# Optimization experiments

Hardware: AMD Instinct MI355X
Metric: run time of the kernel (lower is better)

Reference implementation:

```python
import jax, jax.numpy as jnp
import numpy as np

P = 16; RES = 224; D = 768; L = 12; H = 12; OUT = 512
NP1 = NP2 = RES // P          # 14x14 patches
NTOK = NP1 * NP2 + 1          # 197 tokens (cls + patches)
STD = 5.0                     # gaussian_std for naclip
EPS = 1e-5


def _ln(x, w, b):
    x32 = x.astype(jnp.float32)
    m = x32.mean(-1, keepdims=True)
    v = ((x32 - m) ** 2).mean(-1, keepdims=True)
    return (((x32 - m) * jax.lax.rsqrt(v + EPS)) * w + b).astype(x.dtype)


def _quick_gelu(x):
    return x * jax.nn.sigmoid(1.702 * x)


def _gaussian_addition():
    # VisionTransformer.gaussian_window + get_attention_addition, done analytically:
    # addition[i*NP2+j, k*NP2+l] = window[k-i+NP1-1, l-j+NP2-1]
    w1, w2 = 2 * NP1 - 1, 2 * NP2 - 1
    c = 1.0 / (STD * np.sqrt(2.0))
    k1 = (-(w1 - 1) / 2.0 + np.arange(w1)) * c
    k2 = (-(w2 - 1) / 2.0 + np.arange(w2)) * c
    window = np.exp(-(k1[:, None] ** 2 + k2[None, :] ** 2))
    r = np.arange(NP1)[None, :] - np.arange(NP1)[:, None] + (NP1 - 1)  # [i,k]
    cc = np.arange(NP2)[None, :] - np.arange(NP2)[:, None] + (NP2 - 1)  # [j,l]
    A = window[r[:, None, :, None], cc[None, :, None, :]]  # (NP1,NP2,NP1,NP2)
    A = A.reshape(NP1 * NP2, NP1 * NP2)
    full = np.zeros((NTOK, NTOK), dtype=np.float32)
    full[1:, 1:] = A  # zero row/col for cls token
    return jnp.asarray(full)


def _mha_vanilla(x, wi, bi, wo, bo):
    B, N, _ = x.shape
    hd = D // H
    qkv = x @ wi.T + bi                      # [B,N,3D]
    q, k, v = jnp.split(qkv, 3, axis=-1)
    q = q.reshape(B, N, H, hd); k = k.reshape(B, N, H, hd); v = v.reshape(B, N, H, hd)
    a = jnp.einsum('bqhd,bkhd->bhqk', q, k) * (hd ** -0.5)
    a = jax.nn.softmax(a, axis=-1)
    o = jnp.einsum('bhqk,bkhd->bqhd', a, v).reshape(B, N, D)
    return o @ wo.T + bo


def _mha_naclip(x, wi, bi, wo, bo, addition):
    B, N, _ = x.shape
    hd = D // H
    qkv = x @ wi.T + bi
    _, k, v = jnp.split(qkv, 3, axis=-1)
    k = k.reshape(B, N, H, hd); v = v.reshape(B, N, H, hd)
    a = jnp.einsum('bqhd,bkhd->bhqk', k, k) * (hd ** -0.5) + addition[None, None]
    a = jax.nn.softmax(a, axis=-1)
    o = jnp.einsum('bhqk,bkhd->bqhd', a, v).reshape(B, N, D)
    return o @ wo.T + bo


def _mlp(x, fw, fb, pw, pb):
    return _quick_gelu(x @ fw.T + fb) @ pw.T + pb


def setup_inputs() -> dict:
    key = jax.random.key(0)
    ks = jax.random.split(key, 16)
    s = D ** -0.5
    rn = lambda k, shape, sc=0.02: jax.random.normal(k, shape, jnp.float32) * sc
    return {
        'x': jax.random.normal(ks[0], (32, 3, RES, RES), jnp.float32),
        'conv1_w': rn(ks[1], (D, 3, P, P)),
        'class_embedding': rn(ks[2], (D,), s),
        'pos_embedding': rn(ks[3], (NTOK, D), s),
        'ln_pre_w': jnp.ones((D,)), 'ln_pre_b': jnp.zeros((D,)),
        'in_proj_w': rn(ks[4], (L, 3 * D, D)), 'in_proj_b': rn(ks[5], (L, 3 * D)),
        'out_proj_w': rn(ks[6], (L, D, D)), 'out_proj_b': rn(ks[7], (L, D)),
        'ln1_w': jnp.ones((L, D)), 'ln1_b': jnp.zeros((L, D)),
        'ln2_w': jnp.ones((L, D)), 'ln2_b': jnp.zeros((L, D)),
        'fc_w': rn(ks[8], (L, 4 * D, D)), 'fc_b': rn(ks[9], (L, 4 * D)),
        'cproj_w': rn(ks[10], (L, D, 4 * D)), 'cproj_b': rn(ks[11], (L, D)),
        'ln_post_w': jnp.ones((D,)), 'ln_post_b': jnp.zeros((D,)),
        'proj': rn(ks[12], (D, OUT), s),
    }


def reference(x, conv1_w, class_embedding, pos_embedding, ln_pre_w, ln_pre_b,
              in_proj_w, in_proj_b, out_proj_w, out_proj_b, ln1_w, ln1_b,
              ln2_w, ln2_b, fc_w, fc_b, cproj_w, cproj_b, ln_post_w, ln_post_b, proj):
    B = x.shape[0]
    # patch embed
    h = jax.lax.conv_general_dilated(x, conv1_w, (P, P), 'VALID',
                                     dimension_numbers=('NCHW', 'OIHW', 'NCHW'))
    h = h.reshape(B, D, NP1 * NP2).transpose(0, 2, 1)           # [B,196,D]
    cls = jnp.broadcast_to(class_embedding, (B, 1, D))
    h = jnp.concatenate([cls, h], axis=1) + pos_embedding        # [B,197,D]
    h = _ln(h, ln_pre_w, ln_pre_b)
    addition = _gaussian_addition()
    # first L-1 blocks: vanilla attention
    for i in range(L - 1):
        h = h + _mha_vanilla(_ln(h, ln1_w[i], ln1_b[i]), in_proj_w[i], in_proj_b[i],
                             out_proj_w[i], out_proj_b[i])
        h = h + _mlp(_ln(h, ln2_w[i], ln2_b[i]), fc_w[i], fc_b[i], cproj_w[i], cproj_b[i])
    # last block: naclip key-key attention with gaussian addition (arch='vanilla')
    i = L - 1
    reduced = _mha_naclip(_ln(h, ln1_w[i], ln1_b[i]), in_proj_w[i], in_proj_b[i],
                          out_proj_w[i], out_proj_b[i], addition)
    final = h + reduced
    final = final + _mlp(_ln(final, ln2_w[i], ln2_b[i]), fc_w[i], fc_b[i], cproj_w[i], cproj_b[i])
    return _ln(final, ln_post_w, ln_post_b) @ proj               # [B,197,OUT]
```

## Files before the change

kernel.cpp:

```cpp
#include <hip/hip_runtime.h>
#include <hip/hip_bf16.h>
#include <math.h>

#define BATCH 32
#define NTOK  197
#define NPATCH 196
#define DMODEL 768
#define NLAYER 12
#define NHEAD 12
#define HDIM  64
#define ROWS  (BATCH*NTOK)
#define CROWS (BATCH*NPATCH)
#define DFF   3072
#define DQKV  2304
#define DOUT  512
#define NBH   (BATCH*NHEAD)

#define WOFF_IN   ((size_t)0)
#define WOFF_OUT  ((size_t)(DQKV*DMODEL))
#define WOFF_FC   (WOFF_OUT + (size_t)(DMODEL*DMODEL))
#define WOFF_CP   (WOFF_FC + (size_t)(DFF*DMODEL))
#define WTOT      (WOFF_CP + (size_t)(DMODEL*DFF))

#define WS_H    ((size_t)0)
#define WS_QKVB (WS_H + (size_t)ROWS*DMODEL)
#define WS_GB   (WS_QKVB + (size_t)ROWS*DQKV/2)
#define WS_TB   (WS_GB + (size_t)ROWS*DFF/2)
#define WS_WL   (WS_TB + (size_t)ROWS*DMODEL/2)
#define WS_PTS  (WS_WL + WTOT/2)
#define WS_ADD  (WS_PTS + (size_t)DOUT*DMODEL/2)

typedef unsigned short ushort_t;
typedef __attribute__((ext_vector_type(8))) short bf16x8;
typedef __attribute__((ext_vector_type(4))) float f32x4;

__device__ inline ushort_t bf16rn(float x) {
    uint32_t u = __builtin_bit_cast(uint32_t, x);
    uint32_t r = (u + 0x7FFFu + ((u >> 16) & 1u)) >> 16;
    return (ushort_t)r;
}

#define GLL(src, dst) __builtin_amdgcn_global_load_lds( \
    (const __attribute__((address_space(1))) void*)(src), \
    (__attribute__((address_space(3))) void*)(dst), 16, 0, 0)


__global__ void im2col_bf16_k(const float* __restrict__ x, ushort_t* __restrict__ out) {
    int idx = blockIdx.x * 256 + threadIdx.x;
    if (idx >= CROWS * DMODEL / 4) return;
    int r  = idx / (DMODEL / 4);
    int k4 = (idx - r * (DMODEL / 4)) * 4;
    int b = r / NPATCH, p = r - b * NPATCH;
    int py = p / 14, px = p - py * 14;
    int c = k4 >> 8, rem = k4 & 255, i = rem >> 4, j = rem & 15;
    const float* xp = x + (((size_t)(b * 3 + c) * 224) + py * 16 + i) * 224 + px * 16 + j;
    float4 v = *(const float4*)xp;
    ushort4 hv = {bf16rn(v.x), bf16rn(v.y), bf16rn(v.z), bf16rn(v.w)};
    *(ushort4*)(out + (size_t)r * DMODEL + k4) = hv;
}

__global__ void cvt_w_k(const float* __restrict__ W, ushort_t* __restrict__ out, int NK) {
    int idx = (blockIdx.x * 256 + threadIdx.x) * 4;
    if (idx >= NK) return;
    float4 v = *(const float4*)(W + idx);
    ushort4 hv = {bf16rn(v.x), bf16rn(v.y), bf16rn(v.z), bf16rn(v.w)};
    *(ushort4*)(out + idx) = hv;
}

__global__ void cvt_layer_k(const float* __restrict__ inW, const float* __restrict__ outW,
                            const float* __restrict__ fcW, const float* __restrict__ cpW,
                            ushort_t* __restrict__ wl) {
    size_t idx = ((size_t)blockIdx.x * 256 + threadIdx.x) * 4;
    if (idx >= WTOT) return;
    const float* src; size_t off;
    if (idx < WOFF_OUT)      { src = inW;  off = idx; }
    else if (idx < WOFF_FC)  { src = outW; off = idx - WOFF_OUT; }
    else if (idx < WOFF_CP)  { src = fcW;  off = idx - WOFF_FC; }
    else                     { src = cpW;  off = idx - WOFF_CP; }
    float4 v = *(const float4*)(src + off);
    ushort4 hv = {bf16rn(v.x), bf16rn(v.y), bf16rn(v.z), bf16rn(v.w)};
    *(ushort4*)(wl + idx) = hv;
}

__global__ void cvt_pT_k(const float* __restrict__ proj, ushort_t* __restrict__ out) {
    int idx = blockIdx.x * 256 + threadIdx.x;
    if (idx >= DOUT * DMODEL) return;
    int n = idx / DMODEL, k = idx - n * DMODEL;
    out[(size_t)n * DMODEL + k] = bf16rn(proj[(size_t)k * DOUT + n]);
}

__global__ void embed_k(const float* __restrict__ conv, const float* __restrict__ cls,
                        const float* __restrict__ pos, float* __restrict__ h) {
    int idx = blockIdx.x * 256 + threadIdx.x;
    if (idx >= ROWS * DMODEL) return;
    int r = idx / DMODEL, d = idx - r * DMODEL;
    int b = r / NTOK, tok = r - b * NTOK;
    float v = (tok == 0) ? cls[d] : conv[((size_t)(b * NPATCH + tok - 1)) * DMODEL + d];
    h[idx] = v + pos[(size_t)tok * DMODEL + d];
}

__global__ void gauss_k(float* __restrict__ add) {
    int idx = blockIdx.x * 256 + threadIdx.x;
    if (idx >= NTOK * NTOK) return;
    int i = idx / NTOK, j = idx - i * NTOK;
    float v = 0.f;
    if (i > 0 && j > 0) {
        int p = i - 1, q = j - 1;
        int di = q / 14 - p / 14;
        int dj = q % 14 - p % 14;
        v = expf(-(float)(di * di + dj * dj) * 0.02f);
    }
    add[idx] = v;
}

__global__ __launch_bounds__(256) void ln768_k(const float* __restrict__ in, float* __restrict__ out,
                                               const float* __restrict__ w, const float* __restrict__ b) {
    int row = blockIdx.x, tid = threadIdx.x;
    const float* x = in + (size_t)row * DMODEL;
    float v0 = x[tid], v1 = x[tid + 256], v2 = x[tid + 512];
    float s = v0 + v1 + v2;
    float s2 = v0 * v0 + v1 * v1 + v2 * v2;
    for (int o = 32; o > 0; o >>= 1) { s += __shfl_down(s, o); s2 += __shfl_down(s2, o); }
    __shared__ float red[8];
    int wid = tid >> 6;
    if ((tid & 63) == 0) { red[wid] = s; red[4 + wid] = s2; }
    __syncthreads();
    s  = red[0] + red[1] + red[2] + red[3];
    s2 = red[4] + red[5] + red[6] + red[7];
    float mean = s * (1.0f / 768.0f);
    float var  = s2 * (1.0f / 768.0f) - mean * mean;
    float rinv = rsqrtf(var + 1e-5f);
    float* o_ = out + (size_t)row * DMODEL;
    o_[tid]       = (v0 - mean) * rinv * w[tid]       + b[tid];
    o_[tid + 256] = (v1 - mean) * rinv * w[tid + 256] + b[tid + 256];
    o_[tid + 512] = (v2 - mean) * rinv * w[tid + 512] + b[tid + 512];
}

__global__ __launch_bounds__(256) void ln768_bf16_k(const float* __restrict__ in, ushort_t* __restrict__ out,
                                                    const float* __restrict__ w, const float* __restrict__ b) {
    int row = blockIdx.x, tid = threadIdx.x;
    const float* x = in + (size_t)row * DMODEL;
    float v0 = x[tid], v1 = x[tid + 256], v2 = x[tid + 512];
    float s = v0 + v1 + v2;
    float s2 = v0 * v0 + v1 * v1 + v2 * v2;
    for (int o = 32; o > 0; o >>= 1) { s += __shfl_down(s, o); s2 += __shfl_down(s2, o); }
    __shared__ float red[8];
    int wid = tid >> 6;
    if ((tid & 63) == 0) { red[wid] = s; red[4 + wid] = s2; }
    __syncthreads();
    s  = red[0] + red[1] + red[2] + red[3];
    s2 = red[4] + red[5] + red[6] + red[7];
    float mean = s * (1.0f / 768.0f);
    float var  = s2 * (1.0f / 768.0f) - mean * mean;
    float rinv = rsqrtf(var + 1e-5f);
    ushort_t* o_ = out + (size_t)row * DMODEL;
    o_[tid]       = bf16rn((v0 - mean) * rinv * w[tid]       + b[tid]);
    o_[tid + 256] = bf16rn((v1 - mean) * rinv * w[tid + 256] + b[tid + 256]);
    o_[tid + 512] = bf16rn((v2 - mean) * rinv * w[tid + 512] + b[tid + 512]);
}

__global__ __launch_bounds__(256) void gemm_mfma_k(
    const ushort_t* __restrict__ A, const ushort_t* __restrict__ W,
    const float* __restrict__ bias, float* __restrict__ C, ushort_t* __restrict__ OS,
    int M, int N, int K, int mode)
{
    __shared__ ushort_t As[3][128][32];
    __shared__ ushort_t Bs[3][128][32];
    int tid = threadIdx.x;
    int lane = tid & 63;
    int wave = tid >> 6;
    int wm = wave >> 1, wn = wave & 1;
    int m0 = blockIdx.x * 128, n0 = blockIdx.y * 128;

    int klen = K / gridDim.z;
    int kbeg = blockIdx.z * klen;
    int nt = klen / 32;

    f32x4 acc[4][4];
    #pragma unroll
    for (int i = 0; i < 4; ++i)
        #pragma unroll
        for (int j = 0; j < 4; ++j)
            acc[i][j] = (f32x4){0.f, 0.f, 0.f, 0.f};

    int srow = tid >> 2;
    int skq  = (((tid & 3) ^ ((tid >> 3) & 3)) * 8);
    int ar0 = m0 + srow;      if (ar0 > M - 1) ar0 = M - 1;
    int ar1 = m0 + srow + 64; if (ar1 > M - 1) ar1 = M - 1;
    const ushort_t* Ap0 = A + (size_t)ar0 * K + kbeg + skq;
    const ushort_t* Ap1 = A + (size_t)ar1 * K + kbeg + skq;
    const ushort_t* Wp0 = W + (size_t)(n0 + srow) * K + kbeg + skq;
    const ushort_t* Wp1 = W + (size_t)(n0 + srow + 64) * K + kbeg + skq;
    char* ldsA = (char*)As + tid * 16;
    char* ldsB = (char*)Bs + tid * 16;

    int fr = lane & 15, fq = lane >> 4;
    int rsl = (fq ^ ((fr >> 1) & 3)) * 8;

    #define STAGE(buf_, ko_) do {                         \
        GLL(Ap0 + (ko_), ldsA + (buf_) * 8192);           \
        GLL(Ap1 + (ko_), ldsA + (buf_) * 8192 + 4096);    \
        GLL(Wp0 + (ko_), ldsB + (buf_) * 8192);           \
        GLL(Wp1 + (ko_), ldsB + (buf_) * 8192 + 4096);    \
    } while (0)

    STAGE(0, 0);
    if (nt > 1) STAGE(1, 32);

    for (int t = 0; t < nt; ++t) {
        int cur = t % 3;
        if (t + 1 < nt) {
            asm volatile("s_waitcnt vmcnt(4)" ::: "memory");
        } else {
            asm volatile("s_waitcnt vmcnt(0)" ::: "memory");
        }
        __builtin_amdgcn_s_barrier();
        bf16x8 a[4], b[4];
        #pragma unroll
        for (int fm = 0; fm < 4; ++fm)
            a[fm] = *(const bf16x8*)&As[cur][wm * 64 + fm * 16 + fr][rsl];
        #pragma unroll
        for (int fn = 0; fn < 4; ++fn)
            b[fn] = *(const bf16x8*)&Bs[cur][wn * 64 + fn * 16 + fr][rsl];
        if (t + 2 < nt) STAGE((t + 2) % 3, (size_t)(t + 2) * 32);
        #pragma unroll
        for (int fm = 0; fm < 4; ++fm)
            #pragma unroll
            for (int fn = 0; fn < 4; ++fn)
                acc[fm][fn] = __builtin_amdgcn_mfma_f32_16x16x32_bf16(a[fm], b[fn], acc[fm][fn], 0, 0, 0);
    }
    #undef STAGE

    #pragma unroll
    for (int fn = 0; fn < 4; ++fn) {
        int ccol = n0 + wn * 64 + fn * 16 + fr;
        float bv = bias ? bias[ccol] : 0.f;
        if (mode == 3 && blockIdx.z != 0) bv = 0.f;
        #pragma unroll
        for (int fm = 0; fm < 4; ++fm) {
            int crow0 = m0 + wm * 64 + fm * 16 + fq * 4;
            #pragma unroll
            for (int j = 0; j < 4; ++j) {
                int row = crow0 + j;
                if (row < M) {
                    float v = acc[fm][fn][j] + bv;
                    if (mode == 0) {
                        C[(size_t)row * N + ccol] = v;
                    } else if (mode == 3) {
                        atomicAdd(&C[(size_t)row * N + ccol], v);
                    } else if (mode == 4) {
                        OS[(size_t)row * N + ccol] = bf16rn(v);
                    } else {
                        v = v / (1.0f + expf(-1.702f * v));
                        OS[(size_t)row * N + ccol] = bf16rn(v);
                    }
                }
            }
        }
    }
}

__global__ __launch_bounds__(512, 4) void attn_fused_k(
    const ushort_t* __restrict__ qkvb, ushort_t* __restrict__ out,
    const float* __restrict__ addition, int qoff)
{
    __shared__ ushort_t Ks[208][72];
    __shared__ ushort_t Vt[64][232];
    __shared__ ushort_t Pb[8][2][16][40];
    int tid = threadIdx.x;
    int bh = blockIdx.x;
    int b = bh / NHEAD, hh = bh - b * NHEAD;
    const ushort_t* base = qkvb + (size_t)b * NTOK * DQKV + hh * HDIM;

    int lane = tid & 63, wave = tid >> 6;
    int fr = lane & 15, fq = lane >> 4;
    int qt = blockIdx.y * 8 + wave;

    bf16x8 qf0, qf1;
    if (qt < 13) {
        int qrow = qt * 16 + fr; if (qrow > NTOK - 1) qrow = NTOK - 1;
        const ushort_t* qp = base + (size_t)qrow * DQKV + qoff + fq * 8;
        qf0 = *(const bf16x8*)qp;
        qf1 = *(const bf16x8*)(qp + 32);
    }

    {
        int tt = tid >> 4, dq = tid & 15;
        #pragma unroll
        for (int pass = 0; pass < 7; ++pass) {
            int t = pass * 32 + tt;
            if (t < 208) {
                ushort4 kv = {0, 0, 0, 0}, vv = {0, 0, 0, 0};
                if (t < NTOK) {
                    kv = *(const ushort4*)(base + (size_t)t * DQKV + DMODEL + dq * 4);
                    vv = *(const ushort4*)(base + (size_t)t * DQKV + 2 * DMODEL + dq * 4);
                }
                *(ushort4*)&Ks[t][dq * 4] = kv;
                Vt[dq * 4 + 0][t] = vv.x;
                Vt[dq * 4 + 1][t] = vv.y;
                Vt[dq * 4 + 2][t] = vv.z;
                Vt[dq * 4 + 3][t] = vv.w;
            }
        }
        for (int z = tid; z < 64 * 24; z += 512) Vt[z / 24][208 + z % 24] = 0;
    }
    __syncthreads();

    if (qt < 13) {
        int i0 = qt * 16;
        int irow = i0 + fr; if (irow > NTOK - 1) irow = NTOK - 1;

        f32x4 s[13];
        #pragma unroll
        for (int jt = 0; jt < 13; ++jt) {
            bf16x8 k0 = *(const bf16x8*)&Ks[jt * 16 + fr][fq * 8];
            bf16x8 k1 = *(const bf16x8*)&Ks[jt * 16 + fr][32 + fq * 8];
            f32x4 a = {0.f, 0.f, 0.f, 0.f};
            a = __builtin_amdgcn_mfma_f32_16x16x32_bf16(k0, qf0, a, 0, 0, 0);
            a = __builtin_amdgcn_mfma_f32_16x16x32_bf16(k1, qf1, a, 0, 0, 0);
            s[jt] = a;
        }

        float mx = -1e30f;
        #pragma unroll
        for (int jt = 0; jt < 13; ++jt) {
            int jb = jt * 16 + fq * 4;
            #pragma unroll
            for (int jj = 0; jj < 4; ++jj) {
                int j = jb + jj;
                float v = s[jt][jj] * 0.125f;
                if (addition) v += addition[irow * NTOK + (j < NTOK ? j : NTOK - 1)];
                if (j >= NTOK) v = -1e30f;
                s[jt][jj] = v;
                mx = fmaxf(mx, v);
            }
        }
        mx = fmaxf(mx, __shfl_xor(mx, 16));
        mx = fmaxf(mx, __shfl_xor(mx, 32));
        float sum = 0.f;
        #pragma unroll
        for (int jt = 0; jt < 13; ++jt)
            #pragma unroll
            for (int jj = 0; jj < 4; ++jj) {
                float e = __expf(s[jt][jj] - mx);
                s[jt][jj] = e;
                sum += e;
            }
        sum += __shfl_xor(sum, 16);
        sum += __shfl_xor(sum, 32);
        float inv = 1.0f / sum;

        f32x4 o4[4];
        #pragma unroll
        for (int dt = 0; dt < 4; ++dt) o4[dt] = (f32x4){0.f, 0.f, 0.f, 0.f};

        #define WRITE_P(st_, buf_) do {                                              \
            int jA = 2 * (st_), jB = jA + 1;                                         \
            ushort4 wa = {bf16rn(s[jA][0] * inv), bf16rn(s[jA][1] * inv),            \
                          bf16rn(s[jA][2] * inv), bf16rn(s[jA][3] * inv)};           \
            ushort4 wb = {0, 0, 0, 0};                                               \
            if (jB < 13) wb = (ushort4){bf16rn(s[jB][0] * inv), bf16rn(s[jB][1] * inv), \
                                        bf16rn(s[jB][2] * inv), bf16rn(s[jB][3] * inv)}; \
            *(ushort4*)&Pb[wave][buf_][fr][fq * 4] = wa;                             \
            *(ushort4*)&Pb[wave][buf_][fr][16 + fq * 4] = wb;                        \
        } while (0)

        WRITE_P(0, 0);
        for (int st = 0; st < 7; ++st) {
            asm volatile("s_waitcnt lgkmcnt(0)" ::: "memory");
            bf16x8 pa = *(const bf16x8*)&Pb[wave][st & 1][fr][fq * 8];
            bf16x8 vf0 = *(const bf16x8*)&Vt[0 * 16 + fr][st * 32 + fq * 8];
            bf16x8 vf1 = *(const bf16x8*)&Vt[1 * 16 + fr][st * 32 + fq * 8];
            bf16x8 vf2 = *(const bf16x8*)&Vt[2 * 16 + fr][st * 32 + fq * 8];
            bf16x8 vf3 = *(const bf16x8*)&Vt[3 * 16 + fr][st * 32 + fq * 8];
            if (st < 6) WRITE_P(st + 1, (st + 1) & 1);
            o4[0] = __builtin_amdgcn_mfma_f32_16x16x32_bf16(pa, vf0, o4[0], 0, 0, 0);
            o4[1] = __builtin_amdgcn_mfma_f32_16x16x32_bf16(pa, vf1, o4[1], 0, 0, 0);
            o4[2] = __builtin_amdgcn_mfma_f32_16x16x32_bf16(pa, vf2, o4[2], 0, 0, 0);
            o4[3] = __builtin_amdgcn_mfma_f32_16x16x32_bf16(pa, vf3, o4[3], 0, 0, 0);
        }
        #undef WRITE_P

        #pragma unroll
        for (int jj = 0; jj < 4; ++jj) {
            int ir = i0 + fq * 4 + jj;
            if (ir < NTOK) {
                ushort_t* op = out + ((size_t)(b * NTOK + ir)) * DMODEL + hh * HDIM + fr;
                #pragma unroll
                for (int dt = 0; dt < 4; ++dt)
                    op[dt * 16] = bf16rn(o4[dt][jj]);
            }
        }
    }
}

extern "C" void kernel_launch(void* const* d_in, const int* in_sizes, int n_in,
                              void* d_out, int out_size, void* d_ws, size_t ws_size,
                              hipStream_t stream) {
    const float* x        = (const float*)d_in[0];
    const float* conv1_w  = (const float*)d_in[1];
    const float* cls      = (const float*)d_in[2];
    const float* pos      = (const float*)d_in[3];
    const float* ln_pre_w = (const float*)d_in[4];
    const float* ln_pre_b = (const float*)d_in[5];
    const float* in_proj_w  = (const float*)d_in[6];
    const float* in_proj_b  = (const float*)d_in[7];
    const float* out_proj_w = (const float*)d_in[8];
    const float* out_proj_b = (const float*)d_in[9];
    const float* ln1_w = (const float*)d_in[10];
    const float* ln1_b = (const float*)d_in[11];
    const float* ln2_w = (const float*)d_in[12];
    const float* ln2_b = (const float*)d_in[13];
    const float* fc_w  = (const float*)d_in[14];
    const float* fc_b  = (const float*)d_in[15];
    const float* cproj_w = (const float*)d_in[16];
    const float* cproj_b = (const float*)d_in[17];
    const float* ln_post_w = (const float*)d_in[18];
    const float* ln_post_b = (const float*)d_in[19];
    const float* proj = (const float*)d_in[20];
    float* out = (float*)d_out;

    float* ws   = (float*)d_ws;
    float* h    = ws + WS_H;
    float* ctmp = ws + WS_QKVB;
    ushort_t* qkvb = (ushort_t*)(ws + WS_QKVB);
    ushort_t* gb   = (ushort_t*)(ws + WS_GB);
    ushort_t* tb   = (ushort_t*)(ws + WS_TB);
    ushort_t* wl   = (ushort_t*)(ws + WS_WL);
    ushort_t* pTs  = (ushort_t*)(ws + WS_PTS);
    float* add  = ws + WS_ADD;

    im2col_bf16_k<<<(CROWS * DMODEL / 4 + 255) / 256, 256, 0, stream>>>(x, tb);
    cvt_w_k<<<(DMODEL * DMODEL / 4 + 255) / 256, 256, 0, stream>>>(conv1_w, wl, DMODEL * DMODEL);
    gemm_mfma_k<<<dim3((CROWS + 127) / 128, DMODEL / 128), 256, 0, stream>>>(
        tb, wl, nullptr, ctmp, nullptr, CROWS, DMODEL, DMODEL, 0);
    embed_k<<<(ROWS * DMODEL + 255) / 256, 256, 0, stream>>>(ctmp, cls, pos, h);
    ln768_k<<<ROWS, 256, 0, stream>>>(h, h, ln_pre_w, ln_pre_b);
    gauss_k<<<(NTOK * NTOK + 255) / 256, 256, 0, stream>>>(add);
    cvt_pT_k<<<(DOUT * DMODEL + 255) / 256, 256, 0, stream>>>(proj, pTs);

    const int GY = (ROWS + 127) / 128;
    for (int l = 0; l < NLAYER; ++l) {
        cvt_layer_k<<<(int)(WTOT / 4 / 256), 256, 0, stream>>>(
            in_proj_w + (size_t)l * DQKV * DMODEL, out_proj_w + (size_t)l * DMODEL * DMODEL,
            fc_w + (size_t)l * DFF * DMODEL, cproj_w + (size_t)l * DMODEL * DFF, wl);
        ln768_bf16_k<<<ROWS, 256, 0, stream>>>(h, tb, ln1_w + l * DMODEL, ln1_b + l * DMODEL);
        gemm_mfma_k<<<dim3(GY, DQKV / 128), 256, 0, stream>>>(
            tb, wl + WOFF_IN, in_proj_b + (size_t)l * DQKV, nullptr, qkvb, ROWS, DQKV, DMODEL, 4);
        bool nac = (l == NLAYER - 1);
        attn_fused_k<<<dim3(NBH, 2), 512, 0, stream>>>(qkvb, tb, nac ? add : nullptr, nac ? DMODEL : 0);
        gemm_mfma_k<<<dim3(GY, DMODEL / 128, 2), 256, 0, stream>>>(
            tb, wl + WOFF_OUT, out_proj_b + (size_t)l * DMODEL, h, nullptr, ROWS, DMODEL, DMODEL, 3);
        ln768_bf16_k<<<ROWS, 256, 0, stream>>>(h, tb, ln2_w + l * DMODEL, ln2_b + l * DMODEL);
        gemm_mfma_k<<<dim3(GY, DFF / 128), 256, 0, stream>>>(
            tb, wl + WOFF_FC, fc_b + (size_t)l * DFF, nullptr, gb, ROWS, DFF, DMODEL, 1);
        gemm_mfma_k<<<dim3(GY, DMODEL / 128, 2), 256, 0, stream>>>(
            gb, wl + WOFF_CP, cproj_b + (size_t)l * DMODEL, h, nullptr, ROWS, DMODEL, DFF, 3);
    }

    ln768_bf16_k<<<ROWS, 256, 0, stream>>>(h, tb, ln_post_w, ln_post_b);
    gemm_mfma_k<<<dim3(GY, DOUT / 128), 256, 0, stream>>>(
        tb, pTs, nullptr, out, nullptr, ROWS, DOUT, DMODEL, 0);
}
```

Before: 3.267 ms.

## Batch weight conversion, add 4-deep GEMM pipeline, fuse embed+LN, split-K small GEMMs

```diff
diff --git a/kernel.cpp b/kernel.cpp
--- a/kernel.cpp
+++ b/kernel.cpp
@@ -27,8 +27,6 @@
 #define WS_GB   (WS_QKVB + (size_t)ROWS*DQKV/2)
 #define WS_TB   (WS_GB + (size_t)ROWS*DFF/2)
 #define WS_WL   (WS_TB + (size_t)ROWS*DMODEL/2)
-#define WS_PTS  (WS_WL + WTOT/2)
-#define WS_ADD  (WS_PTS + (size_t)DOUT*DMODEL/2)
 
 typedef unsigned short ushort_t;
 typedef __attribute__((ext_vector_type(8))) short bf16x8;
@@ -82,21 +80,28 @@
     *(ushort4*)(wl + idx) = hv;
 }
 
+__global__ void cvt_all_k(const float* __restrict__ inW, const float* __restrict__ outW,
+                          const float* __restrict__ fcW, const float* __restrict__ cpW,
+                          ushort_t* __restrict__ wl) {
+    size_t idx = ((size_t)blockIdx.x * 256 + threadIdx.x) * 4;
+    if (idx >= (size_t)NLAYER * WTOT) return;
+    int l = (int)(idx / WTOT);
+    size_t off = idx - (size_t)l * WTOT;
+    const float* src; size_t s;
+    if (off < WOFF_OUT)      { src = inW  + (size_t)l * DQKV * DMODEL;  s = off; }
+    else if (off < WOFF_FC)  { src = outW + (size_t)l * DMODEL * DMODEL; s = off - WOFF_OUT; }
+    else if (off < WOFF_CP)  { src = fcW  + (size_t)l * DFF * DMODEL;   s = off - WOFF_FC; }
+    else                     { src = cpW  + (size_t)l * DMODEL * DFF;   s = off - WOFF_CP; }
+    float4 v = *(const float4*)(src + s);
+    ushort4 hv = {bf16rn(v.x), bf16rn(v.y), bf16rn(v.z), bf16rn(v.w)};
+    *(ushort4*)(wl + idx) = hv;
+}
+
 __global__ void cvt_pT_k(const float* __restrict__ proj, ushort_t* __restrict__ out) {
     int idx = blockIdx.x * 256 + threadIdx.x;
     if (idx >= DOUT * DMODEL) return;
     int n = idx / DMODEL, k = idx - n * DMODEL;
     out[(size_t)n * DMODEL + k] = bf16rn(proj[(size_t)k * DOUT + n]);
-}
-
-__global__ void embed_k(const float* __restrict__ conv, const float* __restrict__ cls,
-                        const float* __restrict__ pos, float* __restrict__ h) {
-    int idx = blockIdx.x * 256 + threadIdx.x;
-    if (idx >= ROWS * DMODEL) return;
-    int r = idx / DMODEL, d = idx - r * DMODEL;
-    int b = r / NTOK, tok = r - b * NTOK;
-    float v = (tok == 0) ? cls[d] : conv[((size_t)(b * NPATCH + tok - 1)) * DMODEL + d];
-    h[idx] = v + pos[(size_t)tok * DMODEL + d];
 }
 
 __global__ void gauss_k(float* __restrict__ add) {
@@ -113,13 +118,23 @@
     add[idx] = v;
 }
 
-__global__ __launch_bounds__(256) void ln768_k(const float* __restrict__ in, float* __restrict__ out,
-                                               const float* __restrict__ w, const float* __restrict__ b) {
+__global__ __launch_bounds__(256) void embed_lnpre_k(const float* __restrict__ conv,
+                                                     const float* __restrict__ cls,
+                                                     const float* __restrict__ pos,
+                                                     const float* __restrict__ w,
+                                                     const float* __restrict__ b,
+                                                     float* __restrict__ h) {
     int row = blockIdx.x, tid = threadIdx.x;
-    const float* x = in + (size_t)row * DMODEL;
-    float v0 = x[tid], v1 = x[tid + 256], v2 = x[tid + 512];
-    float s = v0 + v1 + v2;
-    float s2 = v0 * v0 + v1 * v1 + v2 * v2;
+    int bb = row / NTOK, tok = row - bb * NTOK;
+    float e[3];
+    #pragma unroll
+    for (int c = 0; c < 3; ++c) {
+        int d = tid + c * 256;
+        float v = (tok == 0) ? cls[d] : conv[((size_t)(bb * NPATCH + tok - 1)) * DMODEL + d];
+        e[c] = v + pos[(size_t)tok * DMODEL + d];
+    }
+    float s = e[0] + e[1] + e[2];
+    float s2 = e[0]*e[0] + e[1]*e[1] + e[2]*e[2];
     for (int o = 32; o > 0; o >>= 1) { s += __shfl_down(s, o); s2 += __shfl_down(s2, o); }
     __shared__ float red[8];
     int wid = tid >> 6;
@@ -130,10 +145,12 @@
     float mean = s * (1.0f / 768.0f);
     float var  = s2 * (1.0f / 768.0f) - mean * mean;
     float rinv = rsqrtf(var + 1e-5f);
-    float* o_ = out + (size_t)row * DMODEL;
-    o_[tid]       = (v0 - mean) * rinv * w[tid]       + b[tid];
-    o_[tid + 256] = (v1 - mean) * rinv * w[tid + 256] + b[tid + 256];
-    o_[tid + 512] = (v2 - mean) * rinv * w[tid + 512] + b[tid + 512];
+    float* o_ = h + (size_t)row * DMODEL;
+    #pragma unroll
+    for (int c = 0; c < 3; ++c) {
+        int d = tid + c * 256;
+        o_[d] = (e[c] - mean) * rinv * w[d] + b[d];
+    }
 }
 
 __global__ __launch_bounds__(256) void ln768_bf16_k(const float* __restrict__ in, ushort_t* __restrict__ out,
@@ -159,13 +176,14 @@
     o_[tid + 512] = bf16rn((v2 - mean) * rinv * w[tid + 512] + b[tid + 512]);
 }
 
+template<int DEPTH>
 __global__ __launch_bounds__(256) void gemm_mfma_k(
     const ushort_t* __restrict__ A, const ushort_t* __restrict__ W,
     const float* __restrict__ bias, float* __restrict__ C, ushort_t* __restrict__ OS,
     int M, int N, int K, int mode)
 {
-    __shared__ ushort_t As[3][128][32];
-    __shared__ ushort_t Bs[3][128][32];
+    __shared__ ushort_t As[DEPTH][128][32];
+    __shared__ ushort_t Bs[DEPTH][128][32];
     int tid = threadIdx.x;
     int lane = tid & 63;
     int wave = tid >> 6;
@@ -206,15 +224,20 @@
 
     STAGE(0, 0);
     if (nt > 1) STAGE(1, 32);
+    if (DEPTH == 4 && nt > 2) STAGE(2, 64);
 
     for (int t = 0; t < nt; ++t) {
-        int cur = t % 3;
-        if (t + 1 < nt) {
-            asm volatile("s_waitcnt vmcnt(4)" ::: "memory");
+        int cur = t % DEPTH;
+        if constexpr (DEPTH == 3) {
+            if (t + 1 < nt) asm volatile("s_waitcnt vmcnt(4)" ::: "memory");
+            else            asm volatile("s_waitcnt vmcnt(0)" ::: "memory");
         } else {
-            asm volatile("s_waitcnt vmcnt(0)" ::: "memory");
+            if (t + 2 < nt)      asm volatile("s_waitcnt vmcnt(8)" ::: "memory");
+            else if (t + 1 < nt) asm volatile("s_waitcnt vmcnt(4)" ::: "memory");
+            else                 asm volatile("s_waitcnt vmcnt(0)" ::: "memory");
         }
         __builtin_amdgcn_s_barrier();
+        if (t + DEPTH - 1 < nt) STAGE((t + DEPTH - 1) % DEPTH, (size_t)(t + DEPTH - 1) * 32);
         bf16x8 a[4], b[4];
         #pragma unroll
         for (int fm = 0; fm < 4; ++fm)
@@ -222,7 +245,6 @@
         #pragma unroll
         for (int fn = 0; fn < 4; ++fn)
             b[fn] = *(const bf16x8*)&Bs[cur][wn * 64 + fn * 16 + fr][rsl];
-        if (t + 2 < nt) STAGE((t + 2) % 3, (size_t)(t + 2) * 32);
         #pragma unroll
         for (int fm = 0; fm < 4; ++fm)
             #pragma unroll
@@ -427,38 +449,58 @@
     ushort_t* gb   = (ushort_t*)(ws + WS_GB);
     ushort_t* tb   = (ushort_t*)(ws + WS_TB);
     ushort_t* wl   = (ushort_t*)(ws + WS_WL);
-    ushort_t* pTs  = (ushort_t*)(ws + WS_PTS);
-    float* add  = ws + WS_ADD;
+
+    size_t pts_big = WS_WL + (size_t)NLAYER * (WTOT / 2);
+    size_t add_big = pts_big + (size_t)DOUT * DMODEL / 2;
+    size_t need_big = (add_big + (size_t)NTOK * NTOK + 16) * sizeof(float);
+    bool bigws = ws_size >= need_big;
+    size_t pts_off = bigws ? pts_big : (WS_WL + WTOT / 2);
+    size_t add_off = pts_off + (size_t)DOUT * DMODEL / 2;
+    ushort_t* pTs = (ushort_t*)(ws + pts_off);
+    float* add    = ws + add_off;
+
+    ushort_t* convw = gb;
 
     im2col_bf16_k<<<(CROWS * DMODEL / 4 + 255) / 256, 256, 0, stream>>>(x, tb);
-    cvt_w_k<<<(DMODEL * DMODEL / 4 + 255) / 256, 256, 0, stream>>>(conv1_w, wl, DMODEL * DMODEL);
-    gemm_mfma_k<<<dim3((CROWS + 127) / 128, DMODEL / 128), 256, 0, stream>>>(
-        tb, wl, nullptr, ctmp, nullptr, CROWS, DMODEL, DMODEL, 0);
-    embed_k<<<(ROWS * DMODEL + 255) / 256, 256, 0, stream>>>(ctmp, cls, pos, h);
-    ln768_k<<<ROWS, 256, 0, stream>>>(h, h, ln_pre_w, ln_pre_b);
+    cvt_w_k<<<(DMODEL * DMODEL / 4 + 255) / 256, 256, 0, stream>>>(conv1_w, convw, DMODEL * DMODEL);
+    hipMemsetAsync(ctmp, 0, (size_t)CROWS * DMODEL * sizeof(float), stream);
+    gemm_mfma_k<4><<<dim3((CROWS + 127) / 128, DMODEL / 128, 2), 256, 0, stream>>>(
+        tb, convw, nullptr, ctmp, nullptr, CROWS, DMODEL, DMODEL, 3);
+    embed_lnpre_k<<<ROWS, 256, 0, stream>>>(ctmp, cls, pos, ln_pre_w, ln_pre_b, h);
     gauss_k<<<(NTOK * NTOK + 255) / 256, 256, 0, stream>>>(add);
     cvt_pT_k<<<(DOUT * DMODEL + 255) / 256, 256, 0, stream>>>(proj, pTs);
+    if (bigws) {
+        size_t tot = (size_t)NLAYER * WTOT / 4;
+        cvt_all_k<<<(int)((tot + 255) / 256), 256, 0, stream>>>(in_proj_w, out_proj_w, fc_w, cproj_w, wl);
+    }
 
     const int GY = (ROWS + 127) / 128;
     for (int l = 0; l < NLAYER; ++l) {
-        cvt_layer_k<<<(int)(WTOT / 4 / 256), 256, 0, stream>>>(
-            in_proj_w + (size_t)l * DQKV * DMODEL, out_proj_w + (size_t)l * DMODEL * DMODEL,
-            fc_w + (size_t)l * DFF * DMODEL, cproj_w + (size_t)l * DMODEL * DFF, wl);
+        ushort_t* wlp;
+        if (bigws) {
+            wlp = wl + (size_t)l * WTOT;
+        } else {
+            cvt_layer_k<<<(int)(WTOT / 4 / 256), 256, 0, stream>>>(
+                in_proj_w + (size_t)l * DQKV * DMODEL, out_proj_w + (size_t)l * DMODEL * DMODEL,
+                fc_w + (size_t)l * DFF * DMODEL, cproj_w + (size_t)l * DMODEL * DFF, wl);
+            wlp = wl;
+        }
         ln768_bf16_k<<<ROWS, 256, 0, stream>>>(h, tb, ln1_w + l * DMODEL, ln1_b + l * DMODEL);
-        gemm_mfma_k<<<dim3(GY, DQKV / 128), 256, 0, stream>>>(
-            tb, wl + WOFF_IN, in_proj_b + (size_t)l * DQKV, nullptr, qkvb, ROWS, DQKV, DMODEL, 4);
+        gemm_mfma_k<3><<<dim3(GY, DQKV / 128), 256, 0, stream>>>(
+            tb, wlp + WOFF_IN, in_proj_b + (size_t)l * DQKV, nullptr, qkvb, ROWS, DQKV, DMODEL, 4);
         bool nac = (l == NLAYER - 1);
         attn_fused_k<<<dim3(NBH, 2), 512, 0, stream>>>(qkvb, tb, nac ? add : nullptr, nac ? DMODEL : 0);
-        gemm_mfma_k<<<dim3(GY, DMODEL / 128, 2), 256, 0, stream>>>(
-            tb, wl + WOFF_OUT, out_proj_b + (size_t)l * DMODEL, h, nullptr, ROWS, DMODEL, DMODEL, 3);
+        gemm_mfma_k<4><<<dim3(GY, DMODEL / 128, 2), 256, 0, stream>>>(
+            tb, wlp + WOFF_OUT, out_proj_b + (size_t)l * DMODEL, h, nullptr, ROWS, DMODEL, DMODEL, 3);
         ln768_bf16_k<<<ROWS, 256, 0, stream>>>(h, tb, ln2_w + l * DMODEL, ln2_b + l * DMODEL);
-        gemm_mfma_k<<<dim3(GY, DFF / 128), 256, 0, stream>>>(
-            tb, wl + WOFF_FC, fc_b + (size_t)l * DFF, nullptr, gb, ROWS, DFF, DMODEL, 1);
-        gemm_mfma_k<<<dim3(GY, DMODEL / 128, 2), 256, 0, stream>>>(
-            gb, wl + WOFF_CP, cproj_b + (size_t)l * DMODEL, h, nullptr, ROWS, DMODEL, DFF, 3);
+        gemm_mfma_k<3><<<dim3(GY, DFF / 128), 256, 0, stream>>>(
+            tb, wlp + WOFF_FC, fc_b + (size_t)l * DFF, nullptr, gb, ROWS, DFF, DMODEL, 1);
+        gemm_mfma_k<4><<<dim3(GY, DMODEL / 128, 2), 256, 0, stream>>>(
+            gb, wlp + WOFF_CP, cproj_b + (size_t)l * DMODEL, h, nullptr, ROWS, DMODEL, DFF, 3);
     }
 
     ln768_bf16_k<<<ROWS, 256, 0, stream>>>(h, tb, ln_post_w, ln_post_b);
-    gemm_mfma_k<<<dim3(GY, DOUT / 128), 256, 0, stream>>>(
-        tb, pTs, nullptr, out, nullptr, ROWS, DOUT, DMODEL, 0);
-}
+    hipMemsetAsync(out, 0, (size_t)out_size * sizeof(float), stream);
+    gemm_mfma_k<3><<<dim3(GY, DOUT / 128, 4), 256, 0, stream>>>(
+        tb, pTs, nullptr, out, nullptr, ROWS, DOUT, DMODEL, 3);
+}
```

Result: slower. 4.055 ms (+24.1%).
